# Kernel tuning notes

Hardware: AMD Instinct MI355X
Metric: run time of the kernel (lower is better)

## Reference

```python
import jax, jax.numpy as jnp
import numpy as np
from functools import partial

N_NODES = 20000
N_EDGES = 640000
IN_C = 64
HID = 256
OUT_C = 64
HIST = 12
HORIZON = 6


def gcn_conv(x, w, b, src, dst, deg_inv, norm):
    # PyG GCNConv with self loops: out = D^-1/2 (A+I) D^-1/2 (x @ w) + b
    xw = x @ w                                   # [N, H]
    agg = jax.ops.segment_sum(xw[src] * norm[:, None], dst, num_segments=N_NODES)
    return agg + xw * deg_inv[:, None] + b


def gru_cell(x, h, wih, whh, bih, bhh):
    # torch.nn.GRUCell semantics; wih: [3H, in], whh: [3H, H]
    gi = x @ wih.T + bih
    gh = h @ whh.T + bhh
    ir, iz, inn = jnp.split(gi, 3, axis=-1)
    hr, hz, hn = jnp.split(gh, 3, axis=-1)
    r = jax.nn.sigmoid(ir + hr)
    z = jax.nn.sigmoid(iz + hz)
    n = jnp.tanh(inn + r * hn)
    return (1.0 - z) * n + z * h


def setup_inputs() -> dict:
    key = jax.random.key(0)
    ks = jax.random.split(key, 20)
    s = lambda fan: 1.0 / np.sqrt(fan)
    inp = {
        "x_seq": jax.random.normal(ks[0], (1, HIST, N_NODES, IN_C), dtype=jnp.float32),
        "src": jax.random.randint(ks[1], (N_EDGES,), 0, N_NODES),
        "dst": jax.random.randint(ks[2], (N_EDGES,), 0, N_NODES),
        "gcn1_w": jax.random.normal(ks[3], (IN_C, HID), jnp.float32) * s(IN_C),
        "gcn1_b": jnp.zeros((HID,), jnp.float32),
        "gcn2_w": jax.random.normal(ks[4], (HID, HID), jnp.float32) * s(HID),
        "gcn2_b": jnp.zeros((HID,), jnp.float32),
        "proj_w": jax.random.normal(ks[5], (HID, OUT_C), jnp.float32) * s(HID),
        "proj_b": jnp.zeros((OUT_C,), jnp.float32),
    }
    for i, name in enumerate(["gru1", "gru2", "gru3"]):
        k1, k2 = jax.random.split(ks[6 + i])
        inp[f"{name}_wih"] = jax.random.normal(k1, (3 * HID, HID), jnp.float32) * s(HID)
        inp[f"{name}_whh"] = jax.random.normal(k2, (3 * HID, HID), jnp.float32) * s(HID)
        inp[f"{name}_bih"] = jnp.zeros((3 * HID,), jnp.float32)
        inp[f"{name}_bhh"] = jnp.zeros((3 * HID,), jnp.float32)
    return inp


def reference(x_seq, src, dst, gcn1_w, gcn1_b, gcn2_w, gcn2_b, proj_w, proj_b,
              gru1_wih, gru1_whh, gru1_bih, gru1_bhh,
              gru2_wih, gru2_whh, gru2_bih, gru2_bhh,
              gru3_wih, gru3_whh, gru3_bih, gru3_bhh):
    # symmetric GCN normalization with self loops (static graph -> compute once)
    deg = jax.ops.segment_sum(jnp.ones((N_EDGES,), jnp.float32), dst, num_segments=N_NODES) + 1.0
    deg_is = deg ** -0.5
    norm = deg_is[src] * deg_is[dst]   # per-edge norm
    deg_inv = 1.0 / deg                # self-loop norm

    def cell(xt, h1, h2, h3):
        x = jax.nn.relu(gcn_conv(xt, gcn1_w, gcn1_b, src, dst, deg_inv, norm))
        x = jax.nn.relu(gcn_conv(x, gcn2_w, gcn2_b, src, dst, deg_inv, norm))
        h1 = gru_cell(x, h1, gru1_wih, gru1_whh, gru1_bih, gru1_bhh)
        h2 = gru_cell(h1, h2, gru2_wih, gru2_whh, gru2_bih, gru2_bhh)
        h3 = gru_cell(h2, h3, gru3_wih, gru3_whh, gru3_bih, gru3_bhh)
        return h1, h2, h3

    h0 = jnp.zeros((N_NODES, HID), jnp.float32)

    def enc_step(carry, xt):
        return cell(xt, *carry), None

    (h1, h2, h3), _ = jax.lax.scan(enc_step, (h0, h0, h0), x_seq[0])  # [T,N,C]

    def dec_step(carry, _):
        h1, h2, h3, xd = carry
        h1, h2, h3 = cell(xd, h1, h2, h3)
        y = h3 @ proj_w + proj_b       # [N, OUT_C]
        return (h1, h2, h3, y), y

    _, ys = jax.lax.scan(dec_step, (h1, h2, h3, x_seq[0, -1]), None, length=HORIZON)
    return ys[None]  # [1, HORIZON, N, OUT_C]
```

## Files before the change

### kernel.cpp

```cpp
#include <hip/hip_runtime.h>

#define N_NODESC 20000
#define N_EDGESC 640000

typedef _Float16 f16;
typedef __attribute__((ext_vector_type(4))) _Float16 f16x4;
typedef __attribute__((ext_vector_type(8))) _Float16 f16x8;
typedef __attribute__((ext_vector_type(4))) float f32x4;

__device__ __forceinline__ f32x4 mfma16(f16x8 a, f16x8 b, f32x4 c){
  return __builtin_amdgcn_mfma_f32_16x16x32_f16(a, b, c, 0, 0, 0);
}
__device__ __forceinline__ float sigm(float x){ return 1.f/(1.f+__expf(-x)); }
__device__ __forceinline__ float tanh_(float x){
  x = fminf(fmaxf(x, -15.f), 15.f);
  float e = __expf(-2.f*x);
  return (1.f - e)/(1.f + e);
}
__device__ __forceinline__ void stage16(const void* g, void* l){
  __builtin_amdgcn_global_load_lds((const __attribute__((address_space(1))) unsigned int*)g,
                                   (__attribute__((address_space(3))) unsigned int*)l, 16, 0, 0);
}
#define SB       __builtin_amdgcn_sched_barrier(0)
#define AS_VM(n) do{ asm volatile("s_waitcnt vmcnt(" #n ")" ::: "memory"); SB; }while(0)
#define BAR      do{ __builtin_amdgcn_s_barrier(); SB; }while(0)

__global__ __launch_bounds__(256) void k_hist(const int* __restrict__ dst, int* __restrict__ cnt){
  int e = blockIdx.x*256 + threadIdx.x;
  if(e < N_EDGESC) atomicAdd(&cnt[dst[e]], 1);
}

__global__ __launch_bounds__(256) void k_scanA(const int* __restrict__ cnt,
    int* __restrict__ row_ptr, int* __restrict__ btot){
  __shared__ int ws[4];
  int b = blockIdx.x, t = threadIdx.x;
  int i = b*256 + t;
  int v = (i < N_NODESC) ? cnt[i] : 0;
  int lane = t&63, wv = t>>6;
  int incl = v;
  #pragma unroll
  for(int off=1; off<64; off<<=1){ int u = __shfl_up(incl, off); if(lane>=off) incl += u; }
  if(lane==63) ws[wv] = incl;
  __syncthreads();
  int woff = 0;
  for(int k=0;k<wv;k++) woff += ws[k];
  if(i < N_NODESC) row_ptr[i] = woff + incl - v;
  if(t == 255) btot[b] = woff + incl;
}

__global__ __launch_bounds__(128) void k_scanB(const int* __restrict__ btot,
    int* __restrict__ boff, int* __restrict__ row_ptr){
  __shared__ int s[128];
  int t = threadIdx.x;
  int orig = (t < 79) ? btot[t] : 0;
  s[t] = orig;
  __syncthreads();
  #pragma unroll
  for(int off=1; off<128; off<<=1){
    int u = (t>=off) ? s[t-off] : 0;
    __syncthreads();
    s[t] += u;
    __syncthreads();
  }
  if(t < 79) boff[t] = s[t] - orig;
  if(t == 0) row_ptr[N_NODESC] = N_EDGESC;
}

__global__ __launch_bounds__(256) void k_scanC(const int* __restrict__ cnt,
    const int* __restrict__ boff, int* __restrict__ row_ptr,
    float* __restrict__ deg_inv, float* __restrict__ deg_is){
  int i = blockIdx.x*256 + threadIdx.x;
  if(i >= N_NODESC) return;
  row_ptr[i] += boff[blockIdx.x];
  float d = (float)(cnt[i] + 1);
  deg_inv[i] = 1.f/d;
  deg_is[i]  = rsqrtf(d);
}

__global__ __launch_bounds__(256) void k_fill(const int* __restrict__ src, const int* __restrict__ dst,
    const int* __restrict__ row_ptr, int* __restrict__ cursor, const float* __restrict__ deg_is,
    int2* __restrict__ ev){
  int e = blockIdx.x*256 + threadIdx.x;
  if(e >= N_EDGESC) return;
  int d = dst[e], s = src[e];
  int p = atomicAdd(&cursor[d], 1);
  int2 v;
  v.x = s;
  v.y = __float_as_int(deg_is[s]*deg_is[d]);
  ev[row_ptr[d] + p] = v;
}

__global__ __launch_bounds__(256) void k_cvt(const float* __restrict__ x, f16* __restrict__ o, int n4){
  int i = blockIdx.x*256 + threadIdx.x;
  if(i >= n4) return;
  f32x4 v = *(const f32x4*)(x + (size_t)i*4);
  *(f16x4*)(o + (size_t)i*4) = __builtin_convertvector(v, f16x4);
}

__global__ __launch_bounds__(256) void k_pack(const float* __restrict__ w, f16* __restrict__ dstp,
    int K, int NO, int trans){
  int t = blockIdx.x*256 + threadIdx.x;
  if(t >= K*NO) return;
  int i = t&7, g = (t>>3)&3, rest = t>>5;
  int c = rest % NO, kb = rest / NO;
  int k = kb*32 + g*8 + i;
  float v = trans ? w[(size_t)c*K + k] : w[(size_t)k*NO + c];
  dstp[t] = (f16)v;
}

__global__ __launch_bounds__(256) void k_agg64(const f16* __restrict__ x,
    const int* __restrict__ row_ptr, const int2* __restrict__ ev,
    const float* __restrict__ deg_inv, f16* __restrict__ O){
  int n = (blockIdx.x*256 + threadIdx.x)>>6;
  int c = threadIdx.x&63;
  if(n >= N_NODESC) return;
  float acc = deg_inv[n]*(float)x[(size_t)n*64 + c];
  int e0 = row_ptr[n], e1 = row_ptr[n+1];
  int e = e0;
  for(; e+4<=e1; e+=4){
    int2 a=ev[e], b=ev[e+1], cc=ev[e+2], d=ev[e+3];
    float v0=(float)x[(size_t)a.x*64+c],  v1=(float)x[(size_t)b.x*64+c];
    float v2=(float)x[(size_t)cc.x*64+c], v3=(float)x[(size_t)d.x*64+c];
    acc += __int_as_float(a.y)*v0 + __int_as_float(b.y)*v1
         + __int_as_float(cc.y)*v2 + __int_as_float(d.y)*v3;
  }
  for(; e<e1; e++){ int2 a=ev[e]; acc += __int_as_float(a.y)*(float)x[(size_t)a.x*64+c]; }
  O[(size_t)n*64+c] = (f16)acc;
}

__global__ __launch_bounds__(256) void k_agg256(const f16* __restrict__ x1,
    const int* __restrict__ row_ptr, const int2* __restrict__ ev,
    const float* __restrict__ deg_inv, f16* __restrict__ O){
  int n = (blockIdx.x*256 + threadIdx.x)>>6;
  int lane = threadIdx.x&63;
  if(n >= N_NODESC) return;
  const f16x4* xv = (const f16x4*)x1;
  f32x4 acc = __builtin_convertvector(xv[(size_t)n*64 + lane], f32x4) * deg_inv[n];
  int e0 = row_ptr[n], e1 = row_ptr[n+1];
  int e = e0;
  for(; e+4<=e1; e+=4){
    int2 a=ev[e], b=ev[e+1], cc=ev[e+2], d=ev[e+3];
    f32x4 v0=__builtin_convertvector(xv[(size_t)a.x*64+lane],  f32x4);
    f32x4 v1=__builtin_convertvector(xv[(size_t)b.x*64+lane],  f32x4);
    f32x4 v2=__builtin_convertvector(xv[(size_t)cc.x*64+lane], f32x4);
    f32x4 v3=__builtin_convertvector(xv[(size_t)d.x*64+lane],  f32x4);
    acc += v0*__int_as_float(a.y); acc += v1*__int_as_float(b.y);
    acc += v2*__int_as_float(cc.y); acc += v3*__int_as_float(d.y);
  }
  for(; e<e1; e++){ int2 a=ev[e];
    acc += __builtin_convertvector(xv[(size_t)a.x*64+lane], f32x4)*__int_as_float(a.y); }
  ((f16x4*)O)[(size_t)n*64+lane] = __builtin_convertvector(acc, f16x4);
}


__global__ __launch_bounds__(256) void k_gcn1(const f16* __restrict__ A,
    const f16* __restrict__ Bp, const float* __restrict__ bias, f16* __restrict__ C){
  __shared__ f16x8 ldsv[512];
  char* lds = (char*)ldsv;
  const int tid = threadIdx.x, lane = tid&63, w = tid>>6, l15 = lane&15, q = lane>>4;
  const int m0 = blockIdx.x*64;
  #pragma unroll
  for(int i=0;i<2;i++){
    const int o = i*4096 + tid*16;
    const int row = o>>7, s = (o>>4)&7;
    const int c = s ^ (row&7);
    int rgs = m0 + row; if(rgs > N_NODESC-1) rgs = N_NODESC-1;
    stage16((const char*)A + (size_t)rgs*128 + c*16, lds + o);
  }
  AS_VM(0);
  BAR;
  f32x4 acc[4][4];
  #pragma unroll
  for(int rt=0;rt<4;rt++)
    #pragma unroll
    for(int ct=0;ct<4;ct++) acc[rt][ct] = (f32x4){0.f,0.f,0.f,0.f};
  const int l7 = l15&7;
  #pragma unroll
  for(int kb=0;kb<2;kb++){
    f16x8 bf[4];
    #pragma unroll
    for(int ct=0;ct<4;ct++){
      int c = w*64 + ct*16 + l15;
      bf[ct] = *(const f16x8*)(Bp + ((unsigned)(kb*256 + c)*4 + q)*8);
    }
    const int swz = ((kb*4+q) ^ l7)<<4;
    #pragma unroll
    for(int rt=0;rt<4;rt++){
      f16x8 ah = *(const f16x8*)(lds + (rt*16+l15)*128 + swz);
      #pragma unroll
      for(int ct=0;ct<4;ct++)
        acc[rt][ct] = mfma16(ah, bf[ct], acc[rt][ct]);
    }
  }
  #pragma unroll
  for(int rt=0;rt<4;rt++)
    #pragma unroll
    for(int ct=0;ct<4;ct++){
      int c = w*64 + ct*16 + l15;
      float bv = bias[c];
      #pragma unroll
      for(int j=0;j<4;j++){
        int r = m0 + rt*16 + q*4 + j;
        if(r < N_NODESC) C[(size_t)r*256 + c] = (f16)fmaxf(acc[rt][ct][j] + bv, 0.f);
      }
    }
}

__global__ __launch_bounds__(256,3) void k_gcn2(const f16* __restrict__ A,
    const f16* __restrict__ Bp, const float* __restrict__ bias, f16* __restrict__ C){
  __shared__ f16x8 ldsv[2048];
  char* lds = (char*)ldsv;
  const int tid = threadIdx.x, lane = tid&63, w = tid>>6, l15 = lane&15, q = lane>>4;
  const int m0 = blockIdx.x*64;
  #pragma unroll
  for(int i=0;i<8;i++){
    const int o = i*4096 + tid*16;
    const int row = o>>9, s = (o>>4)&31;
    const int c = s ^ (row&7);
    int rgs = m0 + row; if(rgs > N_NODESC-1) rgs = N_NODESC-1;
    stage16((const char*)A + (size_t)rgs*512 + c*16, lds + o);
  }
  f32x4 acc[4][4];
  #pragma unroll
  for(int rt=0;rt<4;rt++)
    #pragma unroll
    for(int ct=0;ct<4;ct++) acc[rt][ct] = (f32x4){0.f,0.f,0.f,0.f};
  f16x8 bf[3][4];
  const int cbase = w*64 + l15;
  #pragma unroll
  for(int s=0;s<2;s++)
    #pragma unroll
    for(int ct=0;ct<4;ct++)
      bf[s][ct] = *(const f16x8*)(Bp + ((unsigned)(s*256 + cbase + ct*16)*4 + q)*8);
  AS_VM(0);
  BAR;
  const int l7 = l15&7;
  #pragma unroll
  for(int kb=0;kb<8;kb++){
    const int s = kb%3;
    if(kb<6){
      const int ns = (kb+2)%3;
      #pragma unroll
      for(int ct=0;ct<4;ct++)
        bf[ns][ct] = *(const f16x8*)(Bp + ((unsigned)((kb+2)*256 + cbase + ct*16)*4 + q)*8);
    }
    const int swz = ((kb*4+q) ^ l7)<<4;
    __builtin_amdgcn_s_setprio(1);
    #pragma unroll
    for(int rt=0;rt<4;rt++){
      f16x8 ah = *(const f16x8*)(lds + (rt*16+l15)*512 + swz);
      #pragma unroll
      for(int ct=0;ct<4;ct++)
        acc[rt][ct] = mfma16(ah, bf[s][ct], acc[rt][ct]);
    }
    __builtin_amdgcn_s_setprio(0);
  }
  #pragma unroll
  for(int rt=0;rt<4;rt++)
    #pragma unroll
    for(int ct=0;ct<4;ct++){
      int c = cbase + ct*16;
      float bv = bias[c];
      #pragma unroll
      for(int j=0;j<4;j++){
        int r = m0 + rt*16 + q*4 + j;
        if(r < N_NODESC) C[(size_t)r*256 + c] = (f16)fmaxf(acc[rt][ct][j] + bv, 0.f);
      }
    }
}

__global__ __launch_bounds__(256,2) void k_gru(
    const f16* __restrict__ X, const f16* __restrict__ H, f16* __restrict__ Nh,
    const f16* __restrict__ Wi, const f16* __restrict__ Wh,
    const float* __restrict__ bih, const float* __restrict__ bhh){
  __shared__ f16x8 ldsv[4096];
  char* lds = (char*)ldsv;
  const int NB = 1252, QQ = NB>>3, RR = NB&7;
  int bid = blockIdx.x;
  int xcd = bid & 7, jj = bid >> 3;
  int nid = (xcd < RR) ? xcd*(QQ+1) + jj : RR*(QQ+1) + (xcd-RR)*QQ + jj;
  const int m0 = (nid>>2)*64;
  const int cb = nid&3;
  const int tid = threadIdx.x, lane = tid&63, w = tid>>6, l15 = lane&15, q = lane>>4;
  const int cc = cb*64 + w*16 + l15;
  const f16* pl[2] = {X, H};
  #pragma unroll
  for(int i=0;i<16;i++){
    const int o = i*4096 + tid*16;
    const int p = o>>15;
    const int rem = o & 32767;
    const int row = rem>>9, s = (rem>>4)&31;
    const int c = s ^ (row&7);
    int rgs = m0 + row; if(rgs > N_NODESC-1) rgs = N_NODESC-1;
    stage16((const char*)pl[p] + (size_t)rgs*512 + c*16, lds + o);
  }
  f32x4 acc[6][4];
  #pragma unroll
  for(int m=0;m<6;m++)
    #pragma unroll
    for(int rt=0;rt<4;rt++) acc[m][rt] = (f32x4){0.f,0.f,0.f,0.f};
  const unsigned wbase = (unsigned)cc*32 + q*8;
  f16x8 bi[3][3], bh[3][3];
  #pragma unroll
  for(int s=0;s<2;s++){
    unsigned wo = wbase + (unsigned)s*24576u;
    bi[s][0] = *(const f16x8*)(Wi + wo);
    bi[s][1] = *(const f16x8*)(Wi + wo + 8192);
    bi[s][2] = *(const f16x8*)(Wi + wo + 16384);
    bh[s][0] = *(const f16x8*)(Wh + wo);
    bh[s][1] = *(const f16x8*)(Wh + wo + 8192);
    bh[s][2] = *(const f16x8*)(Wh + wo + 16384);
  }
  AS_VM(0);
  BAR;
  const int l7 = l15&7;
  #pragma unroll
  for(int kb=0;kb<8;kb++){
    const int s = kb%3;
    if(kb<6){
      const int ns = (kb+2)%3;
      unsigned wo = wbase + (unsigned)(kb+2)*24576u;
      bi[ns][0] = *(const f16x8*)(Wi + wo);
      bi[ns][1] = *(const f16x8*)(Wi + wo + 8192);
      bi[ns][2] = *(const f16x8*)(Wi + wo + 16384);
      bh[ns][0] = *(const f16x8*)(Wh + wo);
      bh[ns][1] = *(const f16x8*)(Wh + wo + 8192);
      bh[ns][2] = *(const f16x8*)(Wh + wo + 16384);
    }
    const int swz = ((kb*4+q) ^ l7)<<4;
    __builtin_amdgcn_s_setprio(1);
    #pragma unroll
    for(int rt=0;rt<4;rt++){
      const int ro = (rt*16+l15)*512 + swz;
      f16x8 ax = *(const f16x8*)(lds + ro);
      f16x8 ah = *(const f16x8*)(lds + 32768 + ro);
      acc[0][rt] = mfma16(ax, bi[s][0], acc[0][rt]);
      acc[1][rt] = mfma16(ax, bi[s][1], acc[1][rt]);
      acc[2][rt] = mfma16(ax, bi[s][2], acc[2][rt]);
      acc[3][rt] = mfma16(ah, bh[s][0], acc[3][rt]);
      acc[4][rt] = mfma16(ah, bh[s][1], acc[4][rt]);
      acc[5][rt] = mfma16(ah, bh[s][2], acc[5][rt]);
    }
    __builtin_amdgcn_s_setprio(0);
  }
  float bir=bih[cc], biz=bih[cc+256], bin=bih[cc+512];
  float bhr=bhh[cc], bhz=bhh[cc+256], bhn=bhh[cc+512];
  const int hcc = (cc>>3);
  const int hlo = (cc&7)*2;
  #pragma unroll
  for(int rt=0;rt<4;rt++){
    #pragma unroll
    for(int j=0;j<4;j++){
      int r = rt*16 + q*4 + j;
      int grow = m0 + r;
      if(grow < N_NODESC){
        float ir=acc[0][rt][j], iz=acc[1][rt][j], in_=acc[2][rt][j];
        float hr=acc[3][rt][j], hz=acc[4][rt][j], hn=acc[5][rt][j];
        float rgt = sigm(ir+bir + hr+bhr);
        float zg = sigm(iz+biz + hz+bhz);
        float ng = tanh_(in_+bin + rgt*(hn+bhn));
        float ho = (float)*(const f16*)(lds + 32768 + r*512 + ((hcc ^ (r&7))<<4) + hlo);
        float v = (1.f-zg)*ng + zg*ho;
        Nh[(size_t)grow*256 + cc] = (f16)v;
      }
    }
  }
}

__global__ __launch_bounds__(256,4) void k_proj(const f16* __restrict__ A,
    const f16* __restrict__ Bp, const float* __restrict__ bias,
    float* __restrict__ C, f16* __restrict__ Cf16){
  __shared__ f16x8 ldsv[2048];
  char* lds = (char*)ldsv;
  const int tid = threadIdx.x, lane = tid&63, w = tid>>6, l15 = lane&15, q = lane>>4;
  const int m0 = blockIdx.x*64;
  const int cc = w*16 + l15;
  #pragma unroll
  for(int i=0;i<8;i++){
    const int o = i*4096 + tid*16;
    const int row = o>>9, s = (o>>4)&31;
    const int c = s ^ (row&7);
    int rgs = m0 + row; if(rgs > N_NODESC-1) rgs = N_NODESC-1;
    stage16((const char*)A + (size_t)rgs*512 + c*16, lds + o);
  }
  f32x4 acc[4];
  #pragma unroll
  for(int rt=0;rt<4;rt++) acc[rt] = (f32x4){0.f,0.f,0.f,0.f};
  f16x8 bf[3];
  bf[0] = *(const f16x8*)(Bp + ((unsigned)(0*64 + cc)*4 + q)*8);
  bf[1] = *(const f16x8*)(Bp + ((unsigned)(1*64 + cc)*4 + q)*8);
  AS_VM(0);
  BAR;
  const int l7 = l15&7;
  #pragma unroll
  for(int kb=0;kb<8;kb++){
    const int s = kb%3;
    if(kb<6)
      bf[(kb+2)%3] = *(const f16x8*)(Bp + ((unsigned)((kb+2)*64 + cc)*4 + q)*8);
    const int swz = ((kb*4+q) ^ l7)<<4;
    #pragma unroll
    for(int rt=0;rt<4;rt++){
      f16x8 ah = *(const f16x8*)(lds + (rt*16+l15)*512 + swz);
      acc[rt] = mfma16(ah, bf[s], acc[rt]);
    }
  }
  #pragma unroll
  for(int rt=0;rt<4;rt++){
    float bv = bias[cc];
    #pragma unroll
    for(int j=0;j<4;j++){
      int r = m0 + rt*16 + q*4 + j;
      if(r < N_NODESC){
        float v = acc[rt][j] + bv;
        C[(size_t)r*64 + cc] = v;
        Cf16[(size_t)r*64 + cc] = (f16)v;
      }
    }
  }
}

extern "C" void kernel_launch(void* const* d_in, const int* in_sizes, int n_in,
                              void* d_out, int out_size, void* d_ws, size_t ws_size,
                              hipStream_t stream){
  const float* x_seq  = (const float*)d_in[0];
  const int*   srcp   = (const int*)  d_in[1];
  const int*   dstp   = (const int*)  d_in[2];
  const float* gcn1_w = (const float*)d_in[3];
  const float* gcn1_b = (const float*)d_in[4];
  const float* gcn2_w = (const float*)d_in[5];
  const float* gcn2_b = (const float*)d_in[6];
  const float* proj_w = (const float*)d_in[7];
  const float* proj_b = (const float*)d_in[8];
  const float* wih[3] = {(const float*)d_in[9],  (const float*)d_in[13], (const float*)d_in[17]};
  const float* whh[3] = {(const float*)d_in[10], (const float*)d_in[14], (const float*)d_in[18]};
  const float* bih[3] = {(const float*)d_in[11], (const float*)d_in[15], (const float*)d_in[19]};
  const float* bhh[3] = {(const float*)d_in[12], (const float*)d_in[16], (const float*)d_in[20]};
  float* out = (float*)d_out;

  const size_t NP = (size_t)N_NODESC*256;
  char* p = (char*)d_ws;
  auto alloc = [&](size_t bytes)->char*{ char* r = p; p += (bytes + 255) & ~(size_t)255; return r; };
  int*   deg_cnt = (int*)  alloc((size_t)2*N_NODESC*4);
  int*   cursor  = deg_cnt + N_NODESC;
  int*   row_ptr = (int*)  alloc((size_t)(N_NODESC+1)*4);
  float* deg_inv = (float*)alloc((size_t)N_NODESC*4);
  float* deg_is  = (float*)alloc((size_t)N_NODESC*4);
  int*   btot    = (int*)  alloc((size_t)128*4);
  int*   boff    = (int*)  alloc((size_t)128*4);
  int2*  ev      = (int2*) alloc((size_t)N_EDGESC*8);
  f16* xf16 = (f16*)alloc((size_t)12*N_NODESC*64*2);
  f16* xdec = (f16*)alloc((size_t)N_NODESC*64*2);
  f16* z64  = (f16*)alloc((size_t)N_NODESC*64*2);
  f16* x1   = (f16*)alloc(NP*2);
  f16* xa   = (f16*)alloc(NP*2);
  f16* hbuf = (f16*)alloc((size_t)2*3*NP*2);
  f16* pk_gcn1 = (f16*)alloc((size_t)64*256*2);
  f16* pk_gcn2 = (f16*)alloc((size_t)256*256*2);
  f16* pk_proj = (f16*)alloc((size_t)256*64*2);
  f16* pk_wi[3]; f16* pk_wh[3];
  for(int i=0;i<3;i++){ pk_wi[i]=(f16*)alloc((size_t)256*768*2); pk_wh[i]=(f16*)alloc((size_t)256*768*2); }

  hipMemsetAsync(deg_cnt, 0, (size_t)2*N_NODESC*4, stream);
  hipMemsetAsync(hbuf,    0, (size_t)3*NP*2, stream);

  k_hist <<<2500,256,0,stream>>>(dstp, deg_cnt);
  k_scanA<<<79,  256,0,stream>>>(deg_cnt, row_ptr, btot);
  k_scanB<<<1,   128,0,stream>>>(btot, boff, row_ptr);
  k_scanC<<<79,  256,0,stream>>>(deg_cnt, boff, row_ptr, deg_inv, deg_is);
  k_fill <<<2500,256,0,stream>>>(srcp, dstp, row_ptr, cursor, deg_is, ev);
  k_cvt  <<<15000,256,0,stream>>>(x_seq, xf16, 12*N_NODESC*64/4);

  k_pack<<<64, 256,0,stream>>>(gcn1_w, pk_gcn1, 64, 256, 0);
  k_pack<<<256,256,0,stream>>>(gcn2_w, pk_gcn2, 256,256, 0);
  k_pack<<<64, 256,0,stream>>>(proj_w, pk_proj, 256, 64, 0);
  for(int i=0;i<3;i++){
    k_pack<<<768,256,0,stream>>>(wih[i], pk_wi[i], 256, 768, 1);
    k_pack<<<768,256,0,stream>>>(whh[i], pk_wh[i], 256, 768, 1);
  }

  auto Hs = [&](int slot, int g)->f16*{ return hbuf + ((size_t)(slot*3+g))*NP; };

  for(int s=0; s<18; s++){
    const f16* xt;
    if(s < 12)       xt = xf16 + (size_t)s*N_NODESC*64;
    else if(s == 12) xt = xf16 + (size_t)11*N_NODESC*64;
    else             xt = xdec;
    int cur = s&1, nxt = cur^1;

    k_agg64 <<<5000,256,0,stream>>>(xt, row_ptr, ev, deg_inv, z64);
    k_gcn1  <<<313, 256,0,stream>>>(z64, pk_gcn1, gcn1_b, x1);
    k_agg256<<<5000,256,0,stream>>>(x1, row_ptr, ev, deg_inv, xa);
    k_gcn2  <<<313, 256,0,stream>>>(xa, pk_gcn2, gcn2_b, xa);

    k_gru<<<1252,256,0,stream>>>(xa,        Hs(cur,0), Hs(nxt,0), pk_wi[0], pk_wh[0], bih[0], bhh[0]);
    k_gru<<<1252,256,0,stream>>>(Hs(nxt,0), Hs(cur,1), Hs(nxt,1), pk_wi[1], pk_wh[1], bih[1], bhh[1]);
    k_gru<<<1252,256,0,stream>>>(Hs(nxt,1), Hs(cur,2), Hs(nxt,2), pk_wi[2], pk_wh[2], bih[2], bhh[2]);

    if(s >= 12)
      k_proj<<<313,256,0,stream>>>(Hs(nxt,2), pk_proj, proj_b, out + (size_t)(s-12)*N_NODESC*64, xdec);
  }
}
```

Baseline: 3.424 ms.

## Widen GCN2/GRU blocks to 512 threads and skip zero-hidden GRU matmul at step 0

k_gcn2 and k_gru now use 512-thread blocks. Each wave in k_gcn2 handles fewer output columns, and each k_gru block covers 128 gate columns instead of 64, which halves the grid and the repeated staging of the X/H tiles. A templated zero-hidden variant of k_gru is used on the first step, where the hidden state is known to be zero. It skips loading and multiplying Wh and H, so the hbuf memset is removed. This trades register pressure and occupancy for less redundant staging, and it depends on the first step never reading hbuf.

```diff
diff --git a/kernel.cpp b/kernel.cpp
--- a/kernel.cpp
+++ b/kernel.cpp
@@ -206,31 +206,31 @@
     }
 }
 
-__global__ __launch_bounds__(256,3) void k_gcn2(const f16* __restrict__ A,
+__global__ __launch_bounds__(512,4) void k_gcn2(const f16* __restrict__ A,
     const f16* __restrict__ Bp, const float* __restrict__ bias, f16* __restrict__ C){
   __shared__ f16x8 ldsv[2048];
   char* lds = (char*)ldsv;
   const int tid = threadIdx.x, lane = tid&63, w = tid>>6, l15 = lane&15, q = lane>>4;
   const int m0 = blockIdx.x*64;
   #pragma unroll
-  for(int i=0;i<8;i++){
-    const int o = i*4096 + tid*16;
+  for(int i=0;i<4;i++){
+    const int o = i*8192 + tid*16;
     const int row = o>>9, s = (o>>4)&31;
     const int c = s ^ (row&7);
     int rgs = m0 + row; if(rgs > N_NODESC-1) rgs = N_NODESC-1;
     stage16((const char*)A + (size_t)rgs*512 + c*16, lds + o);
   }
-  f32x4 acc[4][4];
+  f32x4 acc[4][2];
   #pragma unroll
   for(int rt=0;rt<4;rt++)
     #pragma unroll
-    for(int ct=0;ct<4;ct++) acc[rt][ct] = (f32x4){0.f,0.f,0.f,0.f};
-  f16x8 bf[3][4];
-  const int cbase = w*64 + l15;
+    for(int ct=0;ct<2;ct++) acc[rt][ct] = (f32x4){0.f,0.f,0.f,0.f};
+  f16x8 bf[3][2];
+  const int cbase = w*32 + l15;
   #pragma unroll
   for(int s=0;s<2;s++)
     #pragma unroll
-    for(int ct=0;ct<4;ct++)
+    for(int ct=0;ct<2;ct++)
       bf[s][ct] = *(const f16x8*)(Bp + ((unsigned)(s*256 + cbase + ct*16)*4 + q)*8);
   AS_VM(0);
   BAR;
@@ -241,7 +241,7 @@
     if(kb<6){
       const int ns = (kb+2)%3;
       #pragma unroll
-      for(int ct=0;ct<4;ct++)
+      for(int ct=0;ct<2;ct++)
         bf[ns][ct] = *(const f16x8*)(Bp + ((unsigned)((kb+2)*256 + cbase + ct*16)*4 + q)*8);
     }
     const int swz = ((kb*4+q) ^ l7)<<4;
@@ -250,7 +250,7 @@
     for(int rt=0;rt<4;rt++){
       f16x8 ah = *(const f16x8*)(lds + (rt*16+l15)*512 + swz);
       #pragma unroll
-      for(int ct=0;ct<4;ct++)
+      for(int ct=0;ct<2;ct++)
         acc[rt][ct] = mfma16(ah, bf[s][ct], acc[rt][ct]);
     }
     __builtin_amdgcn_s_setprio(0);
@@ -258,7 +258,7 @@
   #pragma unroll
   for(int rt=0;rt<4;rt++)
     #pragma unroll
-    for(int ct=0;ct<4;ct++){
+    for(int ct=0;ct<2;ct++){
       int c = cbase + ct*16;
       float bv = bias[c];
       #pragma unroll
@@ -269,24 +269,25 @@
     }
 }
 
-__global__ __launch_bounds__(256,2) void k_gru(
+template<int ZH>
+__global__ __launch_bounds__(512,2) void k_gru(
     const f16* __restrict__ X, const f16* __restrict__ H, f16* __restrict__ Nh,
     const f16* __restrict__ Wi, const f16* __restrict__ Wh,
     const float* __restrict__ bih, const float* __restrict__ bhh){
   __shared__ f16x8 ldsv[4096];
   char* lds = (char*)ldsv;
-  const int NB = 1252, QQ = NB>>3, RR = NB&7;
+  const int NB = 626, QQ = NB>>3, RR = NB&7;
   int bid = blockIdx.x;
   int xcd = bid & 7, jj = bid >> 3;
   int nid = (xcd < RR) ? xcd*(QQ+1) + jj : RR*(QQ+1) + (xcd-RR)*QQ + jj;
-  const int m0 = (nid>>2)*64;
-  const int cb = nid&3;
+  const int m0 = (nid>>1)*64;
+  const int cbh = nid&1;
   const int tid = threadIdx.x, lane = tid&63, w = tid>>6, l15 = lane&15, q = lane>>4;
-  const int cc = cb*64 + w*16 + l15;
+  const int cc = cbh*128 + w*16 + l15;
   const f16* pl[2] = {X, H};
   #pragma unroll
-  for(int i=0;i<16;i++){
-    const int o = i*4096 + tid*16;
+  for(int i=0;i<(ZH?4:8);i++){
+    const int o = i*8192 + tid*16;
     const int p = o>>15;
     const int rem = o & 32767;
     const int row = rem>>9, s = (rem>>4)&31;
@@ -307,9 +308,11 @@
     bi[s][0] = *(const f16x8*)(Wi + wo);
     bi[s][1] = *(const f16x8*)(Wi + wo + 8192);
     bi[s][2] = *(const f16x8*)(Wi + wo + 16384);
-    bh[s][0] = *(const f16x8*)(Wh + wo);
-    bh[s][1] = *(const f16x8*)(Wh + wo + 8192);
-    bh[s][2] = *(const f16x8*)(Wh + wo + 16384);
+    if(!ZH){
+      bh[s][0] = *(const f16x8*)(Wh + wo);
+      bh[s][1] = *(const f16x8*)(Wh + wo + 8192);
+      bh[s][2] = *(const f16x8*)(Wh + wo + 16384);
+    }
   }
   AS_VM(0);
   BAR;
@@ -323,9 +326,11 @@
       bi[ns][0] = *(const f16x8*)(Wi + wo);
       bi[ns][1] = *(const f16x8*)(Wi + wo + 8192);
       bi[ns][2] = *(const f16x8*)(Wi + wo + 16384);
-      bh[ns][0] = *(const f16x8*)(Wh + wo);
-      bh[ns][1] = *(const f16x8*)(Wh + wo + 8192);
-      bh[ns][2] = *(const f16x8*)(Wh + wo + 16384);
+      if(!ZH){
+        bh[ns][0] = *(const f16x8*)(Wh + wo);
+        bh[ns][1] = *(const f16x8*)(Wh + wo + 8192);
+        bh[ns][2] = *(const f16x8*)(Wh + wo + 16384);
+      }
     }
     const int swz = ((kb*4+q) ^ l7)<<4;
     __builtin_amdgcn_s_setprio(1);
@@ -333,13 +338,15 @@
     for(int rt=0;rt<4;rt++){
       const int ro = (rt*16+l15)*512 + swz;
       f16x8 ax = *(const f16x8*)(lds + ro);
-      f16x8 ah = *(const f16x8*)(lds + 32768 + ro);
       acc[0][rt] = mfma16(ax, bi[s][0], acc[0][rt]);
       acc[1][rt] = mfma16(ax, bi[s][1], acc[1][rt]);
       acc[2][rt] = mfma16(ax, bi[s][2], acc[2][rt]);
-      acc[3][rt] = mfma16(ah, bh[s][0], acc[3][rt]);
-      acc[4][rt] = mfma16(ah, bh[s][1], acc[4][rt]);
-      acc[5][rt] = mfma16(ah, bh[s][2], acc[5][rt]);
+      if(!ZH){
+        f16x8 ah = *(const f16x8*)(lds + 32768 + ro);
+        acc[3][rt] = mfma16(ah, bh[s][0], acc[3][rt]);
+        acc[4][rt] = mfma16(ah, bh[s][1], acc[4][rt]);
+        acc[5][rt] = mfma16(ah, bh[s][2], acc[5][rt]);
+      }
     }
     __builtin_amdgcn_s_setprio(0);
   }
@@ -355,11 +362,14 @@
       int grow = m0 + r;
       if(grow < N_NODESC){
         float ir=acc[0][rt][j], iz=acc[1][rt][j], in_=acc[2][rt][j];
-        float hr=acc[3][rt][j], hz=acc[4][rt][j], hn=acc[5][rt][j];
+        float hr = ZH ? 0.f : acc[3][rt][j];
+        float hz = ZH ? 0.f : acc[4][rt][j];
+        float hn = ZH ? 0.f : acc[5][rt][j];
         float rgt = sigm(ir+bir + hr+bhr);
         float zg = sigm(iz+biz + hz+bhz);
         float ng = tanh_(in_+bin + rgt*(hn+bhn));
-        float ho = (float)*(const f16*)(lds + 32768 + r*512 + ((hcc ^ (r&7))<<4) + hlo);
+        float ho = ZH ? 0.f
+          : (float)*(const f16*)(lds + 32768 + r*512 + ((hcc ^ (r&7))<<4) + hlo);
         float v = (1.f-zg)*ng + zg*ho;
         Nh[(size_t)grow*256 + cc] = (f16)v;
       }
@@ -461,7 +471,6 @@
   for(int i=0;i<3;i++){ pk_wi[i]=(f16*)alloc((size_t)256*768*2); pk_wh[i]=(f16*)alloc((size_t)256*768*2); }
 
   hipMemsetAsync(deg_cnt, 0, (size_t)2*N_NODESC*4, stream);
-  hipMemsetAsync(hbuf,    0, (size_t)3*NP*2, stream);
 
   k_hist <<<2500,256,0,stream>>>(dstp, deg_cnt);
   k_scanA<<<79,  256,0,stream>>>(deg_cnt, row_ptr, btot);
@@ -490,11 +499,17 @@
     k_agg64 <<<5000,256,0,stream>>>(xt, row_ptr, ev, deg_inv, z64);
     k_gcn1  <<<313, 256,0,stream>>>(z64, pk_gcn1, gcn1_b, x1);
     k_agg256<<<5000,256,0,stream>>>(x1, row_ptr, ev, deg_inv, xa);
-    k_gcn2  <<<313, 256,0,stream>>>(xa, pk_gcn2, gcn2_b, xa);
-
-    k_gru<<<1252,256,0,stream>>>(xa,        Hs(cur,0), Hs(nxt,0), pk_wi[0], pk_wh[0], bih[0], bhh[0]);
-    k_gru<<<1252,256,0,stream>>>(Hs(nxt,0), Hs(cur,1), Hs(nxt,1), pk_wi[1], pk_wh[1], bih[1], bhh[1]);
-    k_gru<<<1252,256,0,stream>>>(Hs(nxt,1), Hs(cur,2), Hs(nxt,2), pk_wi[2], pk_wh[2], bih[2], bhh[2]);
+    k_gcn2  <<<313, 512,0,stream>>>(xa, pk_gcn2, gcn2_b, xa);
+
+    if(s == 0){
+      k_gru<1><<<626,512,0,stream>>>(xa,        Hs(cur,0), Hs(nxt,0), pk_wi[0], pk_wh[0], bih[0], bhh[0]);
+      k_gru<1><<<626,512,0,stream>>>(Hs(nxt,0), Hs(cur,1), Hs(nxt,1), pk_wi[1], pk_wh[1], bih[1], bhh[1]);
+      k_gru<1><<<626,512,0,stream>>>(Hs(nxt,1), Hs(cur,2), Hs(nxt,2), pk_wi[2], pk_wh[2], bih[2], bhh[2]);
+    } else {
+      k_gru<0><<<626,512,0,stream>>>(xa,        Hs(cur,0), Hs(nxt,0), pk_wi[0], pk_wh[0], bih[0], bhh[0]);
+      k_gru<0><<<626,512,0,stream>>>(Hs(nxt,0), Hs(cur,1), Hs(nxt,1), pk_wi[1], pk_wh[1], bih[1], bhh[1]);
+      k_gru<0><<<626,512,0,stream>>>(Hs(nxt,1), Hs(cur,2), Hs(nxt,2), pk_wi[2], pk_wh[2], bih[2], bhh[2]);
+    }
 
     if(s >= 12)
       k_proj<<<313,256,0,stream>>>(Hs(nxt,2), pk_proj, proj_b, out + (size_t)(s-12)*N_NODESC*64, xdec);
```

New measurement: 3.624 ms. 5.8% more time.
